# Kernel tuning notes

Hardware: AMD Instinct MI355X
Metric: run time of the kernel (lower is better)

The kernel has to match this reference:

```python
import jax, jax.numpy as jnp
import numpy as np

N = 50000
E = 800000
IN_DIM, HID, OUT_DIM, HEADS = 256, 128, 64, 4


def _segment_sum(vals, ids, n):
    return jax.ops.segment_sum(vals, ids, num_segments=n)


def gcn_conv(x, src, dst, W, b, n):
    # PyG GCNConv: add self loops, symmetric normalization, aggregate at dst
    xw = x @ W  # [N, HID]
    loop = jnp.arange(n, dtype=src.dtype)
    srcA = jnp.concatenate([src, loop])
    dstA = jnp.concatenate([dst, loop])
    deg = _segment_sum(jnp.ones_like(srcA, dtype=xw.dtype), dstA, n)
    dinv = jnp.where(deg > 0, jax.lax.rsqrt(deg), 0.0)
    norm = dinv[srcA] * dinv[dstA]  # [E+N]
    msg = xw[srcA] * norm[:, None]  # [E+N, HID] -- dominant memory traffic
    return _segment_sum(msg, dstA, n) + b


def layer_norm(h, gamma, beta, eps=1e-5):
    mu = jnp.mean(h, axis=-1, keepdims=True)
    var = jnp.mean(jnp.square(h - mu), axis=-1, keepdims=True)
    return (h - mu) * jax.lax.rsqrt(var + eps) * gamma + beta


def gat_conv(x, src, dst, W, att_src, att_dst, b, n):
    # PyG GATConv (concat=True), self-loops added, eval mode (no dropout)
    xw = (x @ W).reshape(n, HEADS, HID)  # [N, H, C]
    a_s = jnp.sum(xw * att_src, axis=-1)  # [N, H]
    a_d = jnp.sum(xw * att_dst, axis=-1)  # [N, H]
    loop = jnp.arange(n, dtype=src.dtype)
    srcA = jnp.concatenate([src, loop])
    dstA = jnp.concatenate([dst, loop])
    e = jax.nn.leaky_relu(a_s[srcA] + a_d[dstA], 0.2)  # [E+N, H]
    m = jax.ops.segment_max(e, dstA, num_segments=n)  # [N, H]
    ex = jnp.exp(e - m[dstA])
    denom = _segment_sum(ex, dstA, n)  # [N, H] (>=1 entry per node via self loop)
    alpha = ex / denom[dstA]  # [E+N, H]
    msg = xw[srcA] * alpha[:, :, None]  # [E+N, H, C]
    out = _segment_sum(msg, dstA, n)  # [N, H, C]
    return out.reshape(n, HEADS * HID) + b


def setup_inputs() -> dict:
    key = jax.random.key(0)
    ks = jax.random.split(key, 16)
    x = jax.random.normal(ks[0], (N, IN_DIM), dtype=jnp.float32)
    edge_index = jax.random.randint(ks[1], (2, E), 0, N, dtype=jnp.int64)
    s = lambda k, shape, fan: jax.random.normal(k, shape, jnp.float32) / np.sqrt(fan)
    return {
        "x": x,
        "edge_index": edge_index,
        "Win": s(ks[2], (IN_DIM, HID), IN_DIM),
        "bin_": jnp.zeros((HID,), jnp.float32),
        "Wg1": s(ks[3], (HID, HID), HID),
        "bg1": jnp.zeros((HID,), jnp.float32),
        "g1_gamma": jnp.ones((HID,), jnp.float32),
        "g1_beta": jnp.zeros((HID,), jnp.float32),
        "Wg2": s(ks[4], (HID, HID), HID),
        "bg2": jnp.zeros((HID,), jnp.float32),
        "g2_gamma": jnp.ones((HID,), jnp.float32),
        "g2_beta": jnp.zeros((HID,), jnp.float32),
        "Wgat": s(ks[5], (HID, HEADS * HID), HID),
        "att_src": s(ks[6], (HEADS, HID), HID),
        "att_dst": s(ks[7], (HEADS, HID), HID),
        "bgat": jnp.zeros((HEADS * HID,), jnp.float32),
        "Watt_out": s(ks[8], (HEADS * HID, HID), HEADS * HID),
        "batt_out": jnp.zeros((HID,), jnp.float32),
        "Wout": s(ks[9], (HID, OUT_DIM), HID),
        "bout": jnp.zeros((OUT_DIM,), jnp.float32),
    }


def reference(x, edge_index, Win, bin_, Wg1, bg1, g1_gamma, g1_beta,
              Wg2, bg2, g2_gamma, g2_beta, Wgat, att_src, att_dst, bgat,
              Watt_out, batt_out, Wout, bout):
    src, dst = edge_index[0], edge_index[1]
    n = x.shape[0]
    # input projection (dropout = identity in eval)
    h0 = jax.nn.relu(x @ Win + bin_)
    # NOTE: original zip truncates -> only 2 of the 3 GCN layers execute.
    # layer 0 (i==0: no residual)
    h = gcn_conv(h0, src, dst, Wg1, bg1, n)
    h = jax.nn.relu(layer_norm(h, g1_gamma, g1_beta))
    x1 = h
    # layer 1 (i==1: residual)
    h = gcn_conv(x1, src, dst, Wg2, bg2, n)
    h = jax.nn.relu(layer_norm(h, g2_gamma, g2_beta))
    x2 = x1 + h
    # GAT attention block
    a = gat_conv(x2, src, dst, Wgat, att_src, att_dst, bgat, n)
    a = jax.nn.relu(a @ Watt_out + batt_out)
    # output projection
    return a @ Wout + bout
```

## Files before the change

### kernel.cpp

```cpp
#include <hip/hip_runtime.h>
#include <hip/hip_bf16.h>
#include <cstddef>
#include <cstdint>

#define TPB 256
#define HID 128
#define GATD 512
#define HEADS 4

typedef __attribute__((ext_vector_type(8))) short bf16x8;
typedef __attribute__((ext_vector_type(4))) float f32x4;

__device__ __forceinline__ float lrelu02(float x) { return x > 0.0f ? x : 0.2f * x; }

__device__ __forceinline__ unsigned short f2bf_rn(float f) {
  uint32_t u = __float_as_uint(f);
  u += 0x7fff + ((u >> 16) & 1);
  return (unsigned short)(u >> 16);
}
__device__ __forceinline__ float bf2f(unsigned short h) {
  return __uint_as_float(((uint32_t)h) << 16);
}
__device__ __forceinline__ float bflo(uint32_t u) { return __uint_as_float(u << 16); }
__device__ __forceinline__ float bfhi(uint32_t u) { return __uint_as_float(u & 0xffff0000u); }

__global__ void k_zero(int* __restrict__ p, int n) {
  int i = blockIdx.x * blockDim.x + threadIdx.x;
  if (i < n) p[i] = 0;
}

__global__ void k_hist(const int* __restrict__ dst, int* __restrict__ cnt, int E) {
  int i = blockIdx.x * blockDim.x + threadIdx.x;
  if (i < E) atomicAdd(&cnt[dst[i]], 1);
}

__global__ __launch_bounds__(256) void k_scan_blk(const int* __restrict__ cnt,
                                                  int* __restrict__ rowp,
                                                  int* __restrict__ bsum,
                                                  float* __restrict__ dinv, int n) {
  __shared__ int wsum[4];
  const int tid = threadIdx.x, lane = tid & 63, wid = tid >> 6;
  const int base = blockIdx.x * 1024 + tid * 4;
  int v[4];
#pragma unroll
  for (int q = 0; q < 4; ++q) {
    int idx = base + q;
    v[q] = (idx < n) ? cnt[idx] : 0;
    if (idx < n) dinv[idx] = rsqrtf((float)(v[q] + 1));
  }
  int s = v[0] + v[1] + v[2] + v[3];
  int sc = s;
#pragma unroll
  for (int off = 1; off < 64; off <<= 1) {
    int t = __shfl_up(sc, off);
    if (lane >= off) sc += t;
  }
  if (lane == 63) wsum[wid] = sc;
  __syncthreads();
  int woff = 0;
#pragma unroll
  for (int w = 0; w < 4; ++w)
    if (w < wid) woff += wsum[w];
  int run = woff + sc - s;
#pragma unroll
  for (int q = 0; q < 4; ++q) {
    int idx = base + q;
    if (idx < n) rowp[idx] = run;
    run += v[q];
  }
  if (tid == 255) bsum[blockIdx.x] = woff + sc;
}

__global__ __launch_bounds__(256) void k_scan_top(int* __restrict__ bsum, int nb) {
  __shared__ int sm[256];
  const int tid = threadIdx.x;
  int v = (tid < nb) ? bsum[tid] : 0;
  sm[tid] = v;
  __syncthreads();
  for (int off = 1; off < 256; off <<= 1) {
    int t = (tid >= off) ? sm[tid - off] : 0;
    __syncthreads();
    sm[tid] += t;
    __syncthreads();
  }
  int incl = sm[tid];
  if (tid < nb) bsum[tid] = incl - v;
  if (tid == nb - 1) bsum[nb] = incl;
}

__global__ void k_scan_add(int* __restrict__ rowp, const int* __restrict__ bsum,
                           int n, int nb) {
  int i = blockIdx.x * blockDim.x + threadIdx.x;
  if (i < n) rowp[i] += bsum[i >> 10];
  if (i == 0) rowp[n] = bsum[nb];
}

__global__ void k_fill(const int* __restrict__ src, const int* __restrict__ dst,
                       const int* __restrict__ rowp, int* __restrict__ cur,
                       int* __restrict__ colsrc, int E) {
  int i = blockIdx.x * blockDim.x + threadIdx.x;
  if (i < E) {
    int d = dst[i];
    int pos = rowp[d] + atomicAdd(&cur[d], 1);
    colsrc[pos] = src[i];
  }
}

__global__ void k_splitw_all(const float* __restrict__ Win, const float* __restrict__ Wg1,
                             const float* __restrict__ Wg2,
                             unsigned short* __restrict__ WinTh, unsigned short* __restrict__ WinTl,
                             unsigned short* __restrict__ Wg1Th, unsigned short* __restrict__ Wg1Tl,
                             unsigned short* __restrict__ Wg2Th, unsigned short* __restrict__ Wg2Tl) {
  int t = blockIdx.x * blockDim.x + threadIdx.x;
  const float* W;
  unsigned short *H, *L;
  int K, NC, r;
  if (t < 32768)      { W = Win; H = WinTh; L = WinTl; K = 256; NC = 128; r = t; }
  else if (t < 49152) { W = Wg1; H = Wg1Th; L = Wg1Tl; K = 128; NC = 128; r = t - 32768; }
  else if (t < 65536) { W = Wg2; H = Wg2Th; L = Wg2Tl; K = 128; NC = 128; r = t - 49152; }
  else return;
  int k = r / NC, n2 = r % NC;
  float v = W[r];
  unsigned short h = f2bf_rn(v);
  H[(size_t)n2 * K + k] = h;
  L[(size_t)n2 * K + k] = f2bf_rn(v - bf2f(h));
}

__global__ __launch_bounds__(256) void k_prep(const float* __restrict__ Wgat,
                                              const float* __restrict__ att_src,
                                              const float* __restrict__ att_dst,
                                              const float* __restrict__ Wao,
                                              const float* __restrict__ bgat,
                                              const float* __restrict__ bao,
                                              float* __restrict__ waT,
                                              unsigned short* __restrict__ VTh,
                                              unsigned short* __restrict__ VTl,
                                              float* __restrict__ cb) {
  int t = blockIdx.x * blockDim.x + threadIdx.x;
  if (t < 1024) {
    int p = t >> 7, k = t & 127;
    int h = p & 3;
    const float* av = (p < 4 ? att_src : att_dst) + h * HID;
    const float* wrow = Wgat + (size_t)k * GATD + h * HID;
    float s = 0.f;
#pragma unroll 4
    for (int c = 0; c < HID; ++c) s = fmaf(wrow[c], av[c], s);
    waT[t] = s;
  } else if (t < 1024 + 65536) {
    int r = t - 1024;
    int j = r >> 7, k = r & 127;
    int c = j >> 2, h = j & 3;
    const float* wg = Wgat + (size_t)k * GATD + h * HID;
    const float* wa = Wao + (size_t)(h * HID) * HID + c;
    float s = 0.f;
#pragma unroll 4
    for (int d = 0; d < HID; ++d) s = fmaf(wg[d], wa[(size_t)d * HID], s);
    unsigned short hi = f2bf_rn(s);
    VTh[(size_t)j * HID + k] = hi;
    VTl[(size_t)j * HID + k] = f2bf_rn(s - bf2f(hi));
  } else if (t < 1024 + 65536 + 128) {
    int c = t - 1024 - 65536;
    float s = bao[c];
    for (int d = 0; d < GATD; ++d) s = fmaf(bgat[d], Wao[(size_t)d * HID + c], s);
    cb[c] = s;
  }
}

template <int KTOT, int KC, int NCB, bool RELU, bool BIAS, int OUTM, int AMODE>
__global__ __launch_bounds__(256) void k_gemm6(
    const void* __restrict__ Av,
    const unsigned short* __restrict__ BhT, const unsigned short* __restrict__ BlT,
    const float* __restrict__ bias, void* __restrict__ Cv, int M, int NC) {
  constexpr int NSUB = KC / 32;
  constexpr int NCHUNK = KTOT / KC;
  constexpr int NCF = NCB / 16;
  constexpr int UNITS = NSUB * 2 * 4 * NCB;
  __shared__ alignas(16) unsigned short Bs[NSUB][2][4][NCB][8];
  const int tid = threadIdx.x, lane = tid & 63, wid = tid >> 6;
  const int m0 = blockIdx.x * 64;
  const int n0 = blockIdx.y * NCB;
  const int fr = lane & 15, g = lane >> 4;
  const int arow = m0 + wid * 16 + fr;
  const bool aok = arow < M;
  const size_t abase = (size_t)arow * KTOT;

  f32x4 acc[NCF];
#pragma unroll
  for (int cf = 0; cf < NCF; ++cf) acc[cf] = (f32x4){0.f, 0.f, 0.f, 0.f};

  for (int c = 0; c < NCHUNK; ++c) {
    const int c0 = c * KC;
    if (c > 0) __syncthreads();
#pragma unroll
    for (int it = 0; it < UNITS / 256; ++it) {
      const int u = tid + it * 256;
      const int n = u % NCB;
      int rest = u / NCB;
      const int kg = rest & 3;
      rest >>= 2;
      const int p = rest & 1;
      const int sub = rest >> 1;
      const unsigned short* sp =
          (p ? BlT : BhT) + (size_t)(n0 + n) * KTOT + c0 + sub * 32 + kg * 8;
      *(uint4*)&Bs[sub][p][kg][n][0] = *(const uint4*)sp;
    }
    __syncthreads();
#pragma unroll
    for (int sub = 0; sub < NSUB; ++sub) {
      const int kb = c0 + sub * 32 + g * 8;
      bf16x8 a = {};
      if (aok) {
        if (AMODE == 0) {
          a = *(const bf16x8*)((const unsigned short*)Av + abase + kb);
        } else {
          const float* Af = (const float*)Av + abase + kb;
          float4 q0 = *(const float4*)Af;
          float4 q1 = *(const float4*)(Af + 4);
          float av[8] = {q0.x, q0.y, q0.z, q0.w, q1.x, q1.y, q1.z, q1.w};
          union { bf16x8 v; uint32_t u4[4]; } Hu;
#pragma unroll
          for (int q = 0; q < 4; ++q) {
            Hu.u4[q] = (uint32_t)f2bf_rn(av[2 * q]) | ((uint32_t)f2bf_rn(av[2 * q + 1]) << 16);
          }
          a = Hu.v;
        }
      }
#pragma unroll
      for (int cf = 0; cf < NCF; ++cf) {
        bf16x8 b_h = *(const bf16x8*)&Bs[sub][0][g][cf * 16 + fr][0];
        bf16x8 b_l = *(const bf16x8*)&Bs[sub][1][g][cf * 16 + fr][0];
        acc[cf] = __builtin_amdgcn_mfma_f32_16x16x32_bf16(a, b_h, acc[cf], 0, 0, 0);
        acc[cf] = __builtin_amdgcn_mfma_f32_16x16x32_bf16(a, b_l, acc[cf], 0, 0, 0);
      }
    }
  }
#pragma unroll
  for (int cf = 0; cf < NCF; ++cf) {
    const int col = n0 + cf * 16 + fr;
    const float bv = BIAS ? bias[col] : 0.f;
#pragma unroll
    for (int r = 0; r < 4; ++r) {
      const int grow = m0 + wid * 16 + g * 4 + r;
      if (grow < M) {
        float v = acc[cf][r] + bv;
        if (RELU) v = fmaxf(v, 0.f);
        const size_t idx = (size_t)grow * NC + col;
        if (OUTM == 0) ((float*)Cv)[idx] = v;
        else ((unsigned short*)Cv)[idx] = f2bf_rn(v);
      }
    }
  }
}

template <bool L2>
__global__ __launch_bounds__(256) void k_gcn_agg(
    const unsigned short* __restrict__ xwb, const float* __restrict__ dinv,
    const int* __restrict__ rowp, const int* __restrict__ colsrc,
    const float* __restrict__ bias, const float* __restrict__ gamma,
    const float* __restrict__ beta,
    const unsigned short* __restrict__ resb,
    unsigned short* __restrict__ ob,
    const float* __restrict__ waT, float* __restrict__ a_s, float* __restrict__ a_d,
    int n) {
  __shared__ float w[8][HID];
  if (L2) {
    for (int t = threadIdx.x; t < 8 * HID; t += 256) ((float*)w)[t] = waT[t];
    __syncthreads();
  }
  const int lane = threadIdx.x & 63;
  const int i = blockIdx.x * 4 + (threadIdx.x >> 6);
  if (i >= n) return;
  const float di = dinv[i];
  const int c = lane * 2;
  uint32_t v0 = *(const uint32_t*)(xwb + (size_t)i * HID + c);
  float a0 = bflo(v0) * di * di, a1 = bfhi(v0) * di * di;
  float b0 = 0.f, b1 = 0.f;
  const int e0 = rowp[i], e1 = rowp[i + 1];
  int j = e0;
  for (; j + 7 < e1; j += 8) {
    int ss[8];
    float ww[8];
    uint32_t uu[8];
#pragma unroll
    for (int q = 0; q < 8; ++q) ss[q] = colsrc[j + q];
#pragma unroll
    for (int q = 0; q < 8; ++q) ww[q] = dinv[ss[q]] * di;
#pragma unroll
    for (int q = 0; q < 8; ++q) uu[q] = *(const uint32_t*)(xwb + (size_t)ss[q] * HID + c);
#pragma unroll
    for (int q = 0; q < 8; ++q) {
      if (q & 1) {
        b0 = fmaf(bflo(uu[q]), ww[q], b0);
        b1 = fmaf(bfhi(uu[q]), ww[q], b1);
      } else {
        a0 = fmaf(bflo(uu[q]), ww[q], a0);
        a1 = fmaf(bfhi(uu[q]), ww[q], a1);
      }
    }
  }
  for (; j < e1; ++j) {
    int s0 = colsrc[j];
    float w0 = dinv[s0] * di;
    uint32_t u0 = *(const uint32_t*)(xwb + (size_t)s0 * HID + c);
    a0 = fmaf(bflo(u0), w0, a0);
    a1 = fmaf(bfhi(u0), w0, a1);
  }
  a0 += b0;
  a1 += b1;
  a0 += bias[c];
  a1 += bias[c + 1];
  float s1 = a0 + a1, s2 = a0 * a0 + a1 * a1;
#pragma unroll
  for (int m = 32; m >= 1; m >>= 1) {
    s1 += __shfl_xor(s1, m);
    s2 += __shfl_xor(s2, m);
  }
  float mu = s1 * (1.0f / HID);
  float var = s2 * (1.0f / HID) - mu * mu;
  float rstd = rsqrtf(var + 1e-5f);
  float y0 = fmaxf((a0 - mu) * rstd * gamma[c] + beta[c], 0.0f);
  float y1 = fmaxf((a1 - mu) * rstd * gamma[c + 1] + beta[c + 1], 0.0f);
  if (L2) {
    uint32_t rb = *(const uint32_t*)(resb + (size_t)i * HID + c);
    y0 += bflo(rb);
    y1 += bfhi(rb);
  }
  *(uint32_t*)(ob + (size_t)i * HID + c) =
      (uint32_t)f2bf_rn(y0) | ((uint32_t)f2bf_rn(y1) << 16);
  if (L2) {
    float p[8];
#pragma unroll
    for (int h = 0; h < 8; ++h) p[h] = y0 * w[h][c] + y1 * w[h][c + 1];
#pragma unroll
    for (int m = 32; m >= 1; m >>= 1) {
#pragma unroll
      for (int h = 0; h < 8; ++h) p[h] += __shfl_xor(p[h], m);
    }
    if (lane == 0) {
      a_s[i * 4 + 0] = p[0]; a_s[i * 4 + 1] = p[1];
      a_s[i * 4 + 2] = p[2]; a_s[i * 4 + 3] = p[3];
      a_d[i * 4 + 0] = p[4]; a_d[i * 4 + 1] = p[5];
      a_d[i * 4 + 2] = p[6]; a_d[i * 4 + 3] = p[7];
    }
  }
}

__global__ __launch_bounds__(512) void k_gat_agg3(const unsigned short* __restrict__ zb,
                                                  const float* __restrict__ a_s,
                                                  const float* __restrict__ a_d,
                                                  const int* __restrict__ rowp,
                                                  const int* __restrict__ colsrc,
                                                  const float* __restrict__ cb,
                                                  const float* __restrict__ Wout,
                                                  const float* __restrict__ bout,
                                                  float* __restrict__ outp,
                                                  int n) {
  __shared__ float4 albuf[8][64];
  __shared__ int sbuf[8][64];
  __shared__ float attbuf[8][HID];
  __shared__ float Wlds[HID * 64];
  for (int t = threadIdx.x; t < HID * 64 / 4; t += 512)
    *(float4*)&Wlds[t * 4] = *(const float4*)&Wout[t * 4];
  __syncthreads();
  const int lane = threadIdx.x & 63;
  const int wid = threadIdx.x >> 6;
  const int i = blockIdx.x * 8 + wid;
  if (i >= n) return;
  const float4 adv = *(const float4*)(a_d + i * 4);
  const float4 asv = *(const float4*)(a_s + i * 4);
  float es0 = lrelu02(asv.x + adv.x);
  float es1 = lrelu02(asv.y + adv.y);
  float es2 = lrelu02(asv.z + adv.z);
  float es3 = lrelu02(asv.w + adv.w);
  const int e0 = rowp[i], e1 = rowp[i + 1];
  float m0 = es0, m1 = es1, m2 = es2, m3 = es3;
  for (int j = e0 + lane; j < e1; j += 64) {
    int s = colsrc[j];
    const float4 av = *(const float4*)(a_s + s * 4);
    m0 = fmaxf(m0, lrelu02(av.x + adv.x));
    m1 = fmaxf(m1, lrelu02(av.y + adv.y));
    m2 = fmaxf(m2, lrelu02(av.z + adv.z));
    m3 = fmaxf(m3, lrelu02(av.w + adv.w));
  }
#pragma unroll
  for (int m = 32; m >= 1; m >>= 1) {
    m0 = fmaxf(m0, __shfl_xor(m0, m));
    m1 = fmaxf(m1, __shfl_xor(m1, m));
    m2 = fmaxf(m2, __shfl_xor(m2, m));
    m3 = fmaxf(m3, __shfl_xor(m3, m));
  }
  float d0 = 0.f, d1 = 0.f, d2 = 0.f, d3 = 0.f;
  for (int j = e0 + lane; j < e1; j += 64) {
    int s = colsrc[j];
    const float4 av = *(const float4*)(a_s + s * 4);
    d0 += __expf(lrelu02(av.x + adv.x) - m0);
    d1 += __expf(lrelu02(av.y + adv.y) - m1);
    d2 += __expf(lrelu02(av.z + adv.z) - m2);
    d3 += __expf(lrelu02(av.w + adv.w) - m3);
  }
#pragma unroll
  for (int m = 32; m >= 1; m >>= 1) {
    d0 += __shfl_xor(d0, m);
    d1 += __shfl_xor(d1, m);
    d2 += __shfl_xor(d2, m);
    d3 += __shfl_xor(d3, m);
  }
  d0 += __expf(es0 - m0);
  d1 += __expf(es1 - m1);
  d2 += __expf(es2 - m2);
  d3 += __expf(es3 - m3);
  const float inv0 = 1.0f / d0, inv1 = 1.0f / d1, inv2 = 1.0f / d2, inv3 = 1.0f / d3;
  const float4 asf = make_float4(__expf(es0 - m0) * inv0, __expf(es1 - m1) * inv1,
                                 __expf(es2 - m2) * inv2, __expf(es3 - m3) * inv3);
  const int col8 = lane * 8;
  uint4 u = *(const uint4*)(zb + (size_t)i * GATD + col8);
  float4 accC0 = make_float4(bflo(u.x) * asf.x, bfhi(u.x) * asf.y,
                             bflo(u.y) * asf.z, bfhi(u.y) * asf.w);
  float4 accC1 = make_float4(bflo(u.z) * asf.x, bfhi(u.z) * asf.y,
                             bflo(u.w) * asf.z, bfhi(u.w) * asf.w);
  for (int b = e0; b < e1; b += 64) {
    int j = b + lane;
    if (j < e1) {
      int s = colsrc[j];
      const float4 av = *(const float4*)(a_s + s * 4);
      albuf[wid][lane] = make_float4(__expf(lrelu02(av.x + adv.x) - m0) * inv0,
                                     __expf(lrelu02(av.y + adv.y) - m1) * inv1,
                                     __expf(lrelu02(av.z + adv.z) - m2) * inv2,
                                     __expf(lrelu02(av.w + adv.w) - m3) * inv3);
      sbuf[wid][lane] = s;
    }
    asm volatile("s_waitcnt lgkmcnt(0)" ::: "memory");
    const int cnt = min(64, e1 - b);
    for (int t = 0; t < cnt; ++t) {
      float4 a4 = albuf[wid][t];
      int s = sbuf[wid][t];
      uint4 w = *(const uint4*)(zb + (size_t)s * GATD + col8);
      accC0.x = fmaf(bflo(w.x), a4.x, accC0.x);
      accC0.y = fmaf(bfhi(w.x), a4.y, accC0.y);
      accC0.z = fmaf(bflo(w.y), a4.z, accC0.z);
      accC0.w = fmaf(bfhi(w.y), a4.w, accC0.w);
      accC1.x = fmaf(bflo(w.z), a4.x, accC1.x);
      accC1.y = fmaf(bfhi(w.z), a4.y, accC1.y);
      accC1.z = fmaf(bflo(w.w), a4.z, accC1.z);
      accC1.w = fmaf(bfhi(w.w), a4.w, accC1.w);
    }
  }
  const int c0 = lane * 2;
  float2 cbv = *(const float2*)(cb + c0);
  float o0 = fmaxf(accC0.x + accC0.y + accC0.z + accC0.w + cbv.x, 0.0f);
  float o1 = fmaxf(accC1.x + accC1.y + accC1.z + accC1.w + cbv.y, 0.0f);
  attbuf[wid][c0] = o0;
  attbuf[wid][c0 + 1] = o1;
  asm volatile("s_waitcnt lgkmcnt(0)" ::: "memory");
  float acc = bout[lane];
#pragma unroll 16
  for (int c = 0; c < HID; ++c) acc = fmaf(attbuf[wid][c], Wlds[c * 64 + lane], acc);
  outp[(size_t)i * 64 + lane] = acc;
}

extern "C" void kernel_launch(void* const* d_in, const int* in_sizes, int n_in,
                              void* d_out, int out_size, void* d_ws, size_t ws_size,
                              hipStream_t stream) {
  const float* x = (const float*)d_in[0];
  const int* ei = (const int*)d_in[1];
  const float* Win = (const float*)d_in[2];
  const float* bin = (const float*)d_in[3];
  const float* Wg1 = (const float*)d_in[4];
  const float* bg1 = (const float*)d_in[5];
  const float* g1g = (const float*)d_in[6];
  const float* g1b = (const float*)d_in[7];
  const float* Wg2 = (const float*)d_in[8];
  const float* bg2 = (const float*)d_in[9];
  const float* g2g = (const float*)d_in[10];
  const float* g2b = (const float*)d_in[11];
  const float* Wgat = (const float*)d_in[12];
  const float* att_s = (const float*)d_in[13];
  const float* att_d = (const float*)d_in[14];
  const float* bgat = (const float*)d_in[15];
  const float* Wao = (const float*)d_in[16];
  const float* bao = (const float*)d_in[17];
  const float* Wout = (const float*)d_in[18];
  const float* bout = (const float*)d_in[19];

  const int N = in_sizes[0] / 256;
  const int E = in_sizes[1] / 2;
  const int* src = ei;
  const int* dst = ei + E;

  char* base = (char*)d_ws;
  size_t off = 0;
  unsigned short* h0b = (unsigned short*)(base + off); off += (size_t)N * HID * 2;
  unsigned short* x1b = (unsigned short*)(base + off); off += (size_t)N * HID * 2;
  unsigned short* xwb = (unsigned short*)(base + off); off += (size_t)N * HID * 2;
  unsigned short* x2b = (unsigned short*)(base + off); off += (size_t)N * HID * 2;
  unsigned short* zb = (unsigned short*)(base + off); off += (size_t)N * GATD * 2;
  float* dinv = (float*)(base + off);                 off += (size_t)N * 4;
  float* a_s = (float*)(base + off);                  off += (size_t)N * 16;
  float* a_d = (float*)(base + off);                  off += (size_t)N * 16;
  float* waT = (float*)(base + off);                  off += 4096;
  float* cb = (float*)(base + off);                   off += 512;
  unsigned short *WinTh, *WinTl, *Wg1Th, *Wg1Tl, *Wg2Th, *Wg2Tl, *VTh, *VTl;
  WinTh = (unsigned short*)(base + off); off += 256 * 128 * 2;
  WinTl = (unsigned short*)(base + off); off += 256 * 128 * 2;
  Wg1Th = (unsigned short*)(base + off); off += 128 * 128 * 2;
  Wg1Tl = (unsigned short*)(base + off); off += 128 * 128 * 2;
  Wg2Th = (unsigned short*)(base + off); off += 128 * 128 * 2;
  Wg2Tl = (unsigned short*)(base + off); off += 128 * 128 * 2;
  VTh = (unsigned short*)(base + off);   off += 512 * 128 * 2;
  VTl = (unsigned short*)(base + off);   off += 512 * 128 * 2;
  int* rowp = (int*)(base + off);   off += (size_t)(N + 1) * 4;
  int* colsrc = (int*)(base + off); off += (size_t)E * 4;
  const int nb2 = (N + 1023) / 1024;
  int* bsum = (int*)(base + off);   off += (size_t)(nb2 + 2) * 4;
  int* cnt = (int*)zb;
  int* cur = cnt + N;

  const int eb = (E + TPB - 1) / TPB;
  const int zbk = (2 * N + TPB - 1) / TPB;
  const int ab = (N + 3) / 4;
  const int ab8 = (N + 7) / 8;
  const int gm = (N + 63) / 64;

  k_zero<<<zbk, TPB, 0, stream>>>(cnt, 2 * N);
  k_hist<<<eb, TPB, 0, stream>>>(dst, cnt, E);
  k_scan_blk<<<nb2, 256, 0, stream>>>(cnt, rowp, bsum, dinv, N);
  k_scan_top<<<1, 256, 0, stream>>>(bsum, nb2);
  k_scan_add<<<(N + 255) / 256, 256, 0, stream>>>(rowp, bsum, N, nb2);
  k_fill<<<eb, TPB, 0, stream>>>(src, dst, rowp, cur, colsrc, E);
  k_prep<<<(1024 + 65536 + 128 + 255) / 256, 256, 0, stream>>>(
      Wgat, att_s, att_d, Wao, bgat, bao, waT, VTh, VTl, cb);
  k_splitw_all<<<(65536 + 255) / 256, 256, 0, stream>>>(
      Win, Wg1, Wg2, WinTh, WinTl, Wg1Th, Wg1Tl, Wg2Th, Wg2Tl);

  k_gemm6<256, 64, 128, true, true, 1, 1><<<dim3(gm, 1), 256, 0, stream>>>(
      x, WinTh, WinTl, bin, h0b, N, 128);
  k_gemm6<128, 64, 128, false, false, 1, 0><<<dim3(gm, 1), 256, 0, stream>>>(
      h0b, Wg1Th, Wg1Tl, nullptr, xwb, N, 128);
  k_gcn_agg<false><<<ab, 256, 0, stream>>>(xwb, dinv, rowp, colsrc, bg1, g1g, g1b,
                                           nullptr, x1b, nullptr, nullptr, nullptr, N);
  k_gemm6<128, 64, 128, false, false, 1, 0><<<dim3(gm, 1), 256, 0, stream>>>(
      x1b, Wg2Th, Wg2Tl, nullptr, xwb, N, 128);
  k_gcn_agg<true><<<ab, 256, 0, stream>>>(xwb, dinv, rowp, colsrc, bg2, g2g, g2b,
                                          x1b, x2b, waT, a_s, a_d, N);
  k_gemm6<128, 32, 256, false, false, 1, 0><<<dim3(gm, 2), 256, 0, stream>>>(
      x2b, VTh, VTl, nullptr, zb, N, 512);
  k_gat_agg3<<<ab8, 512, 0, stream>>>(zb, a_s, a_d, rowp, colsrc, cb, Wout, bout,
                                      (float*)d_out, N);
}
```

Baseline: 476.8 us.

## Aggregate raw x2 per head before projecting, then GEMM through fused GAT-out weights

The GAT block now gathers 128-wide bf16 x2 rows per edge instead of 512-wide projected rows. It accumulates per-head weighted sums into a 512-wide buffer, then applies the fused Wgat·Watt_out projection as a K=512 GEMM with bias and ReLU. The final Wout projection moves from an in-kernel LDS loop to a separate split-bf16 GEMM. This cuts per-edge gather traffic by about 4x, at the cost of writing and reading an extra N×512 intermediate and one more kernel launch.

```diff
diff --git a/kernel.cpp b/kernel.cpp
--- a/kernel.cpp
+++ b/kernel.cpp
@@ -107,17 +107,19 @@
 }
 
 __global__ void k_splitw_all(const float* __restrict__ Win, const float* __restrict__ Wg1,
-                             const float* __restrict__ Wg2,
+                             const float* __restrict__ Wg2, const float* __restrict__ Wout,
                              unsigned short* __restrict__ WinTh, unsigned short* __restrict__ WinTl,
                              unsigned short* __restrict__ Wg1Th, unsigned short* __restrict__ Wg1Tl,
-                             unsigned short* __restrict__ Wg2Th, unsigned short* __restrict__ Wg2Tl) {
+                             unsigned short* __restrict__ Wg2Th, unsigned short* __restrict__ Wg2Tl,
+                             unsigned short* __restrict__ WoutTh, unsigned short* __restrict__ WoutTl) {
   int t = blockIdx.x * blockDim.x + threadIdx.x;
   const float* W;
   unsigned short *H, *L;
   int K, NC, r;
-  if (t < 32768)      { W = Win; H = WinTh; L = WinTl; K = 256; NC = 128; r = t; }
-  else if (t < 49152) { W = Wg1; H = Wg1Th; L = Wg1Tl; K = 128; NC = 128; r = t - 32768; }
-  else if (t < 65536) { W = Wg2; H = Wg2Th; L = Wg2Tl; K = 128; NC = 128; r = t - 49152; }
+  if (t < 32768)      { W = Win;  H = WinTh;  L = WinTl;  K = 256; NC = 128; r = t; }
+  else if (t < 49152) { W = Wg1;  H = Wg1Th;  L = Wg1Tl;  K = 128; NC = 128; r = t - 32768; }
+  else if (t < 65536) { W = Wg2;  H = Wg2Th;  L = Wg2Tl;  K = 128; NC = 128; r = t - 49152; }
+  else if (t < 73728) { W = Wout; H = WoutTh; L = WoutTl; K = 128; NC = 64;  r = t - 65536; }
   else return;
   int k = r / NC, n2 = r % NC;
   float v = W[r];
@@ -133,8 +135,8 @@
                                               const float* __restrict__ bgat,
                                               const float* __restrict__ bao,
                                               float* __restrict__ waT,
-                                              unsigned short* __restrict__ VTh,
-                                              unsigned short* __restrict__ VTl,
+                                              unsigned short* __restrict__ V2Th,
+                                              unsigned short* __restrict__ V2Tl,
                                               float* __restrict__ cb) {
   int t = blockIdx.x * blockDim.x + threadIdx.x;
   if (t < 1024) {
@@ -156,8 +158,8 @@
 #pragma unroll 4
     for (int d = 0; d < HID; ++d) s = fmaf(wg[d], wa[(size_t)d * HID], s);
     unsigned short hi = f2bf_rn(s);
-    VTh[(size_t)j * HID + k] = hi;
-    VTl[(size_t)j * HID + k] = f2bf_rn(s - bf2f(hi));
+    V2Th[(size_t)c * GATD + k * 4 + h] = hi;
+    V2Tl[(size_t)c * GATD + k * 4 + h] = f2bf_rn(s - bf2f(hi));
   } else if (t < 1024 + 65536 + 128) {
     int c = t - 1024 - 65536;
     float s = bao[c];
@@ -345,26 +347,18 @@
   }
 }
 
-__global__ __launch_bounds__(512) void k_gat_agg3(const unsigned short* __restrict__ zb,
+__global__ __launch_bounds__(256) void k_gat_agg4(const unsigned short* __restrict__ x2b,
                                                   const float* __restrict__ a_s,
                                                   const float* __restrict__ a_d,
                                                   const int* __restrict__ rowp,
                                                   const int* __restrict__ colsrc,
-                                                  const float* __restrict__ cb,
-                                                  const float* __restrict__ Wout,
-                                                  const float* __restrict__ bout,
-                                                  float* __restrict__ outp,
+                                                  unsigned short* __restrict__ ub,
                                                   int n) {
-  __shared__ float4 albuf[8][64];
-  __shared__ int sbuf[8][64];
-  __shared__ float attbuf[8][HID];
-  __shared__ float Wlds[HID * 64];
-  for (int t = threadIdx.x; t < HID * 64 / 4; t += 512)
-    *(float4*)&Wlds[t * 4] = *(const float4*)&Wout[t * 4];
-  __syncthreads();
+  __shared__ float4 albuf[4][64];
+  __shared__ int sbuf[4][64];
   const int lane = threadIdx.x & 63;
   const int wid = threadIdx.x >> 6;
-  const int i = blockIdx.x * 8 + wid;
+  const int i = blockIdx.x * 4 + wid;
   if (i >= n) return;
   const float4 adv = *(const float4*)(a_d + i * 4);
   const float4 asv = *(const float4*)(a_s + i * 4);
@@ -412,12 +406,11 @@
   const float inv0 = 1.0f / d0, inv1 = 1.0f / d1, inv2 = 1.0f / d2, inv3 = 1.0f / d3;
   const float4 asf = make_float4(__expf(es0 - m0) * inv0, __expf(es1 - m1) * inv1,
                                  __expf(es2 - m2) * inv2, __expf(es3 - m3) * inv3);
-  const int col8 = lane * 8;
-  uint4 u = *(const uint4*)(zb + (size_t)i * GATD + col8);
-  float4 accC0 = make_float4(bflo(u.x) * asf.x, bfhi(u.x) * asf.y,
-                             bflo(u.y) * asf.z, bfhi(u.y) * asf.w);
-  float4 accC1 = make_float4(bflo(u.z) * asf.x, bfhi(u.z) * asf.y,
-                             bflo(u.w) * asf.z, bfhi(u.w) * asf.w);
+  const int c0 = lane * 2;
+  uint32_t sv = *(const uint32_t*)(x2b + (size_t)i * HID + c0);
+  float x0 = bflo(sv), x1 = bfhi(sv);
+  float4 A0 = make_float4(x0 * asf.x, x0 * asf.y, x0 * asf.z, x0 * asf.w);
+  float4 A1 = make_float4(x1 * asf.x, x1 * asf.y, x1 * asf.z, x1 * asf.w);
   for (int b = e0; b < e1; b += 64) {
     int j = b + lane;
     if (j < e1) {
@@ -434,28 +427,20 @@
     for (int t = 0; t < cnt; ++t) {
       float4 a4 = albuf[wid][t];
       int s = sbuf[wid][t];
-      uint4 w = *(const uint4*)(zb + (size_t)s * GATD + col8);
-      accC0.x = fmaf(bflo(w.x), a4.x, accC0.x);
-      accC0.y = fmaf(bfhi(w.x), a4.y, accC0.y);
-      accC0.z = fmaf(bflo(w.y), a4.z, accC0.z);
-      accC0.w = fmaf(bfhi(w.y), a4.w, accC0.w);
-      accC1.x = fmaf(bflo(w.z), a4.x, accC1.x);
-      accC1.y = fmaf(bfhi(w.z), a4.y, accC1.y);
-      accC1.z = fmaf(bflo(w.w), a4.z, accC1.z);
-      accC1.w = fmaf(bfhi(w.w), a4.w, accC1.w);
-    }
-  }
-  const int c0 = lane * 2;
-  float2 cbv = *(const float2*)(cb + c0);
-  float o0 = fmaxf(accC0.x + accC0.y + accC0.z + accC0.w + cbv.x, 0.0f);
-  float o1 = fmaxf(accC1.x + accC1.y + accC1.z + accC1.w + cbv.y, 0.0f);
-  attbuf[wid][c0] = o0;
-  attbuf[wid][c0 + 1] = o1;
-  asm volatile("s_waitcnt lgkmcnt(0)" ::: "memory");
-  float acc = bout[lane];
-#pragma unroll 16
-  for (int c = 0; c < HID; ++c) acc = fmaf(attbuf[wid][c], Wlds[c * 64 + lane], acc);
-  outp[(size_t)i * 64 + lane] = acc;
+      uint32_t wv = *(const uint32_t*)(x2b + (size_t)s * HID + c0);
+      float w0 = bflo(wv), w1 = bfhi(wv);
+      A0.x = fmaf(w0, a4.x, A0.x); A0.y = fmaf(w0, a4.y, A0.y);
+      A0.z = fmaf(w0, a4.z, A0.z); A0.w = fmaf(w0, a4.w, A0.w);
+      A1.x = fmaf(w1, a4.x, A1.x); A1.y = fmaf(w1, a4.y, A1.y);
+      A1.z = fmaf(w1, a4.z, A1.z); A1.w = fmaf(w1, a4.w, A1.w);
+    }
+  }
+  uint4 o;
+  o.x = (uint32_t)f2bf_rn(A0.x) | ((uint32_t)f2bf_rn(A0.y) << 16);
+  o.y = (uint32_t)f2bf_rn(A0.z) | ((uint32_t)f2bf_rn(A0.w) << 16);
+  o.z = (uint32_t)f2bf_rn(A1.x) | ((uint32_t)f2bf_rn(A1.y) << 16);
+  o.w = (uint32_t)f2bf_rn(A1.z) | ((uint32_t)f2bf_rn(A1.w) << 16);
+  *(uint4*)(ub + (size_t)i * GATD + lane * 8) = o;
 }
 
 extern "C" void kernel_launch(void* const* d_in, const int* in_sizes, int n_in,
@@ -493,32 +478,35 @@
   unsigned short* x1b = (unsigned short*)(base + off); off += (size_t)N * HID * 2;
   unsigned short* xwb = (unsigned short*)(base + off); off += (size_t)N * HID * 2;
   unsigned short* x2b = (unsigned short*)(base + off); off += (size_t)N * HID * 2;
-  unsigned short* zb = (unsigned short*)(base + off); off += (size_t)N * GATD * 2;
+  unsigned short* ub = (unsigned short*)(base + off); off += (size_t)N * GATD * 2;
+  unsigned short* attb = h0b;
   float* dinv = (float*)(base + off);                 off += (size_t)N * 4;
   float* a_s = (float*)(base + off);                  off += (size_t)N * 16;
   float* a_d = (float*)(base + off);                  off += (size_t)N * 16;
   float* waT = (float*)(base + off);                  off += 4096;
   float* cb = (float*)(base + off);                   off += 512;
-  unsigned short *WinTh, *WinTl, *Wg1Th, *Wg1Tl, *Wg2Th, *Wg2Tl, *VTh, *VTl;
+  unsigned short *WinTh, *WinTl, *Wg1Th, *Wg1Tl, *Wg2Th, *Wg2Tl, *V2Th, *V2Tl;
+  unsigned short *WoutTh, *WoutTl;
   WinTh = (unsigned short*)(base + off); off += 256 * 128 * 2;
   WinTl = (unsigned short*)(base + off); off += 256 * 128 * 2;
   Wg1Th = (unsigned short*)(base + off); off += 128 * 128 * 2;
   Wg1Tl = (unsigned short*)(base + off); off += 128 * 128 * 2;
   Wg2Th = (unsigned short*)(base + off); off += 128 * 128 * 2;
   Wg2Tl = (unsigned short*)(base + off); off += 128 * 128 * 2;
-  VTh = (unsigned short*)(base + off);   off += 512 * 128 * 2;
-  VTl = (unsigned short*)(base + off);   off += 512 * 128 * 2;
+  V2Th = (unsigned short*)(base + off);  off += 512 * 128 * 2;
+  V2Tl = (unsigned short*)(base + off);  off += 512 * 128 * 2;
+  WoutTh = (unsigned short*)(base + off); off += 128 * 64 * 2;
+  WoutTl = (unsigned short*)(base + off); off += 128 * 64 * 2;
   int* rowp = (int*)(base + off);   off += (size_t)(N + 1) * 4;
   int* colsrc = (int*)(base + off); off += (size_t)E * 4;
   const int nb2 = (N + 1023) / 1024;
   int* bsum = (int*)(base + off);   off += (size_t)(nb2 + 2) * 4;
-  int* cnt = (int*)zb;
+  int* cnt = (int*)ub;
   int* cur = cnt + N;
 
   const int eb = (E + TPB - 1) / TPB;
   const int zbk = (2 * N + TPB - 1) / TPB;
   const int ab = (N + 3) / 4;
-  const int ab8 = (N + 7) / 8;
   const int gm = (N + 63) / 64;
 
   k_zero<<<zbk, TPB, 0, stream>>>(cnt, 2 * N);
@@ -528,9 +516,9 @@
   k_scan_add<<<(N + 255) / 256, 256, 0, stream>>>(rowp, bsum, N, nb2);
   k_fill<<<eb, TPB, 0, stream>>>(src, dst, rowp, cur, colsrc, E);
   k_prep<<<(1024 + 65536 + 128 + 255) / 256, 256, 0, stream>>>(
-      Wgat, att_s, att_d, Wao, bgat, bao, waT, VTh, VTl, cb);
-  k_splitw_all<<<(65536 + 255) / 256, 256, 0, stream>>>(
-      Win, Wg1, Wg2, WinTh, WinTl, Wg1Th, Wg1Tl, Wg2Th, Wg2Tl);
+      Wgat, att_s, att_d, Wao, bgat, bao, waT, V2Th, V2Tl, cb);
+  k_splitw_all<<<(73728 + 255) / 256, 256, 0, stream>>>(
+      Win, Wg1, Wg2, Wout, WinTh, WinTl, Wg1Th, Wg1Tl, Wg2Th, Wg2Tl, WoutTh, WoutTl);
 
   k_gemm6<256, 64, 128, true, true, 1, 1><<<dim3(gm, 1), 256, 0, stream>>>(
       x, WinTh, WinTl, bin, h0b, N, 128);
@@ -542,8 +530,9 @@
       x1b, Wg2Th, Wg2Tl, nullptr, xwb, N, 128);
   k_gcn_agg<true><<<ab, 256, 0, stream>>>(xwb, dinv, rowp, colsrc, bg2, g2g, g2b,
                                           x1b, x2b, waT, a_s, a_d, N);
-  k_gemm6<128, 32, 256, false, false, 1, 0><<<dim3(gm, 2), 256, 0, stream>>>(
-      x2b, VTh, VTl, nullptr, zb, N, 512);
-  k_gat_agg3<<<ab8, 512, 0, stream>>>(zb, a_s, a_d, rowp, colsrc, cb, Wout, bout,
-                                      (float*)d_out, N);
-}
+  k_gat_agg4<<<ab, 256, 0, stream>>>(x2b, a_s, a_d, rowp, colsrc, ub, N);
+  k_gemm6<512, 64, 128, true, true, 1, 0><<<dim3(gm, 1), 256, 0, stream>>>(
+      ub, V2Th, V2Tl, cb, attb, N, 128);
+  k_gemm6<128, 128, 64, false, true, 0, 0><<<dim3(gm, 1), 256, 0, stream>>>(
+      attb, WoutTh, WoutTl, bout, (float*)d_out, N, 64);
+}
```

Result: faster. 419.1 us (-12.1%).
